# Performance work log

Measured on AMD Instinct MI355X. Metric: run time of the kernel, lower is better.

The kernel has to match this reference:

```python
import jax, jax.numpy as jnp
import numpy as np

EPS_NORM = 1e-6
EPS_LN = 1e-5


def setup_inputs() -> dict:
    key = jax.random.key(0)
    ks = jax.random.split(key, 6)
    b, m, d = 8, 1024, 768
    n, p = 64, 16
    h = 2 * d
    x = jax.random.normal(ks[0], (b, m, d), dtype=jnp.float32)
    phi = jax.random.normal(ks[1], (n, p, d), dtype=jnp.float32)
    # per-expert LayerNorm affine params
    ln_g = jnp.ones((n, d), dtype=jnp.float32)
    ln_b = jnp.zeros((n, d), dtype=jnp.float32)
    # per-expert MLP weights (torch Linear default init ~ U(-1/sqrt(fan_in), ...); use scaled normal)
    w1 = jax.random.normal(ks[2], (n, d, h), dtype=jnp.float32) * (1.0 / np.sqrt(d))
    b1 = jax.random.normal(ks[3], (n, h), dtype=jnp.float32) * 0.01
    w2 = jax.random.normal(ks[4], (n, h, d), dtype=jnp.float32) * (1.0 / np.sqrt(h))
    b2 = jax.random.normal(ks[5], (n, d), dtype=jnp.float32) * 0.01
    return {"x": x, "phi": phi, "ln_g": ln_g, "ln_b": ln_b,
            "w1": w1, "b1": b1, "w2": w2, "b2": b2}


def _layernorm(x, g, b):
    mu = jnp.mean(x, axis=-1, keepdims=True)
    var = jnp.mean(jnp.square(x - mu), axis=-1, keepdims=True)
    return (x - mu) * jax.lax.rsqrt(var + EPS_LN) * g + b


def reference(x, phi, ln_g, ln_b, w1, b1, w2, b2):
    # normalize phi over axis=0 (expert axis), as in the torch __init__
    phi_n = phi * jax.lax.rsqrt(jnp.sum(jnp.square(phi), axis=0, keepdims=True) + EPS_NORM)
    bsz, m, d = x.shape
    n, p, _ = phi_n.shape
    # routing logits: [b, m, n, p]
    logits = jnp.einsum('bmd,npd->bmnp', x, phi_n)
    # dispatch: softmax over tokens m
    D = jax.nn.softmax(logits, axis=1)
    # combine: softmax over flattened slots (n*p)
    C = jax.nn.softmax(logits.reshape(bsz, m, n * p), axis=-1)
    # input slots: [b, n, p, d]
    Xs = jnp.einsum('bmd,bmnp->bnpd', x, D)
    # batched per-expert MLP: LN -> Linear -> GELU -> Linear
    hdn = _layernorm(Xs, ln_g[:, None, :], ln_b[:, None, :])
    hdn = jnp.einsum('bnpd,ndh->bnph', hdn, w1) + b1[:, None, :]
    hdn = jax.nn.gelu(hdn, approximate=False)
    Ys = jnp.einsum('bnph,nhd->bnpd', hdn, w2) + b2[:, None, :]
    # combine: [b, m, d]
    Ys = Ys.reshape(bsz, n * p, d)
    Y = jnp.einsum('bsd,bms->bmd', Ys, C)
    return Y
```

## Files before the change

kernel.cpp:

```cpp
#include <hip/hip_runtime.h>
#include <math.h>

#define B 8
#define M 1024
#define D 768
#define NEXP 64
#define P 16
#define H 1536
#define S 1024
#define EPS_NORM 1e-6f
#define EPS_LN   1e-5f

typedef unsigned short u16;
typedef __attribute__((ext_vector_type(8))) short bf16x8;
typedef __attribute__((ext_vector_type(4))) float f32x4;

__device__ __forceinline__ u16 f2bf(float f) {
    union { float f; unsigned u; } v; v.f = f;
    unsigned r = v.u + 0x7FFFu + ((v.u >> 16) & 1u);
    return (u16)(r >> 16);
}

__device__ __forceinline__ float gelu_exact(float x) {
    return 0.5f * x * (1.0f + erff(x * 0.70710678118654752440f));
}

#define GLL16(g, l) __builtin_amdgcn_global_load_lds( \
    (const __attribute__((address_space(1))) void*)(g), \
    (__attribute__((address_space(3))) void*)(l), 16, 0, 0)

__device__ __forceinline__ void mfma_core_128(const u16* __restrict__ Ag,
                                              const u16* __restrict__ Bg,
                                              int K, u16* As, u16* Bs,
                                              f32x4 (&acc)[4][4]) {
    const int t    = threadIdx.x;
    const int lane = t & 63;
    const int wave = t >> 6;
    const int wr   = (wave >> 1) << 6;
    const int wc   = (wave & 1) << 6;
    const int quad = lane >> 4;
    const int l16  = lane & 15;
    const u16* ga0 = Ag + (size_t)(t >> 2) * K + (t & 3) * 8;
    const u16* ga1 = ga0 + (size_t)64 * K;
    const u16* gb0 = Bg + (size_t)(t >> 2) * K + (t & 3) * 8;
    const u16* gb1 = gb0 + (size_t)64 * K;
    u16* la0 = As + t * 8;
    u16* la1 = la0 + 2048;
    u16* lb0 = Bs + t * 8;
    u16* lb1 = lb0 + 2048;
    const u16* arp = As + (wr + l16) * 32 + quad * 8;
    const u16* brp = Bs + (wc + l16) * 32 + quad * 8;
    for (int k0 = 0; k0 < K; k0 += 32) {
        __syncthreads();
        GLL16(ga0 + k0, la0);
        GLL16(ga1 + k0, la1);
        GLL16(gb0 + k0, lb0);
        GLL16(gb1 + k0, lb1);
        __syncthreads();
        bf16x8 af[4], bfr[4];
#pragma unroll
        for (int i = 0; i < 4; ++i) af[i]  = *(const bf16x8*)(arp + i * 512);
#pragma unroll
        for (int j = 0; j < 4; ++j) bfr[j] = *(const bf16x8*)(brp + j * 512);
#pragma unroll
        for (int i = 0; i < 4; ++i)
#pragma unroll
            for (int j = 0; j < 4; ++j)
                acc[i][j] = __builtin_amdgcn_mfma_f32_16x16x32_bf16(af[i], bfr[j], acc[i][j], 0, 0, 0);
    }
}

#define EPI_VARS \
    const int t = threadIdx.x; const int lane = t & 63; const int wave = t >> 6; \
    const int wr = (wave >> 1) << 6; const int wc = (wave & 1) << 6; \
    const int quad = lane >> 4; const int l16 = lane & 15; (void)t;


__global__ __launch_bounds__(256) void cvt_x_kernel(const float* __restrict__ x,
                                                    u16* __restrict__ xb) {
    size_t i = ((size_t)blockIdx.x * 256 + threadIdx.x) * 4;
    float4 v = *(const float4*)(x + i);
    ushort4 o;
    o.x = f2bf(v.x); o.y = f2bf(v.y); o.z = f2bf(v.z); o.w = f2bf(v.w);
    *(ushort4*)(xb + i) = o;
}

__global__ __launch_bounds__(256) void phi_norm_kernel(const float* __restrict__ phi,
                                                       u16* __restrict__ phinb) {
    int pos = blockIdx.x * 256 + threadIdx.x;
    float ss = 0.f;
#pragma unroll 4
    for (int nn = 0; nn < NEXP; ++nn) {
        float v = phi[nn * (P*D) + pos];
        ss += v * v;
    }
    float r = rsqrtf(ss + EPS_NORM);
#pragma unroll 4
    for (int nn = 0; nn < NEXP; ++nn)
        phinb[nn * (P*D) + pos] = f2bf(phi[nn * (P*D) + pos] * r);
}

__global__ __launch_bounds__(256) void transpose_cvt_kernel(const float* __restrict__ in,
                                                            u16* __restrict__ out,
                                                            int R, int C,
                                                            size_t inStride, size_t outStride) {
    __shared__ float tile[64][65];
    const float* inb = in + (size_t)blockIdx.z * inStride;
    u16* outb = out + (size_t)blockIdx.z * outStride;
    int r0 = blockIdx.y * 64, c0 = blockIdx.x * 64;
    int tt = threadIdx.x;
    int rr = tt >> 4, c4 = (tt & 15) * 4;
#pragma unroll
    for (int i = 0; i < 4; ++i) {
        float4 v = *(const float4*)(inb + (size_t)(r0 + rr + i*16) * C + c0 + c4);
        tile[rr + i*16][c4 + 0] = v.x;
        tile[rr + i*16][c4 + 1] = v.y;
        tile[rr + i*16][c4 + 2] = v.z;
        tile[rr + i*16][c4 + 3] = v.w;
    }
    __syncthreads();
    int cr = tt >> 4, r4 = (tt & 15) * 4;
#pragma unroll
    for (int i = 0; i < 4; ++i) {
        int crow = cr + i * 16;
        ushort4 o;
        o.x = f2bf(tile[r4 + 0][crow]);
        o.y = f2bf(tile[r4 + 1][crow]);
        o.z = f2bf(tile[r4 + 2][crow]);
        o.w = f2bf(tile[r4 + 3][crow]);
        *(ushort4*)(outb + (size_t)(c0 + crow) * R + r0 + r4) = o;
    }
}


__global__ __launch_bounds__(256) void gemm_logits_mfma(const u16* __restrict__ xb,
                                                        const u16* __restrict__ phinb,
                                                        float* __restrict__ logits) {
    __shared__ __align__(16) u16 As[4096], Bs[4096];
    f32x4 acc[4][4];
#pragma unroll
    for (int i = 0; i < 4; ++i)
#pragma unroll
        for (int j = 0; j < 4; ++j) acc[i][j] = (f32x4){0.f, 0.f, 0.f, 0.f};
    const int row0 = blockIdx.y * 128, col0 = blockIdx.x * 128;
    mfma_core_128(xb + (size_t)row0 * D, phinb + (size_t)col0 * D, D, As, Bs, acc);
    EPI_VARS;
#pragma unroll
    for (int i = 0; i < 4; ++i)
#pragma unroll
        for (int j = 0; j < 4; ++j) {
            int col = col0 + wc + j*16 + l16;
#pragma unroll
            for (int r = 0; r < 4; ++r) {
                int row = row0 + wr + i*16 + quad*4 + r;
                logits[(size_t)row * S + col] = acc[i][j][r];
            }
        }
}

__global__ __launch_bounds__(256) void gemm_dispatch_mfma(const u16* __restrict__ DT,
                                                          const u16* __restrict__ xT,
                                                          float* __restrict__ Xs) {
    __shared__ __align__(16) u16 As[4096], Bs[4096];
    f32x4 acc[4][4];
#pragma unroll
    for (int i = 0; i < 4; ++i)
#pragma unroll
        for (int j = 0; j < 4; ++j) acc[i][j] = (f32x4){0.f, 0.f, 0.f, 0.f};
    const int b = blockIdx.z;
    const int row0 = blockIdx.y * 128, col0 = blockIdx.x * 128;
    mfma_core_128(DT + ((size_t)b * S + row0) * M,
                  xT + ((size_t)b * D + col0) * M, M, As, Bs, acc);
    EPI_VARS;
#pragma unroll
    for (int i = 0; i < 4; ++i)
#pragma unroll
        for (int j = 0; j < 4; ++j) {
            int col = col0 + wc + j*16 + l16;
#pragma unroll
            for (int r = 0; r < 4; ++r) {
                int row = row0 + wr + i*16 + quad*4 + r;
                Xs[((size_t)b * S + row) * D + col] = acc[i][j][r];
            }
        }
}

__global__ __launch_bounds__(256) void gemm_mlp1_mfma(const u16* __restrict__ hdnE,
                                                      const u16* __restrict__ w1T,
                                                      const float* __restrict__ b1,
                                                      u16* __restrict__ h1) {
    __shared__ __align__(16) u16 As[4096], Bs[4096];
    f32x4 acc[4][4];
#pragma unroll
    for (int i = 0; i < 4; ++i)
#pragma unroll
        for (int j = 0; j < 4; ++j) acc[i][j] = (f32x4){0.f, 0.f, 0.f, 0.f};
    const int n = blockIdx.z;
    const int col0 = blockIdx.x * 128;
    mfma_core_128(hdnE + (size_t)n * 128 * D,
                  w1T + ((size_t)n * H + col0) * D, D, As, Bs, acc);
    EPI_VARS;
#pragma unroll
    for (int i = 0; i < 4; ++i)
#pragma unroll
        for (int j = 0; j < 4; ++j) {
            int h = col0 + wc + j*16 + l16;
            float bias = b1[n * H + h];
#pragma unroll
            for (int r = 0; r < 4; ++r) {
                int row = wr + i*16 + quad*4 + r;
                h1[((size_t)n * 128 + row) * H + h] = f2bf(gelu_exact(acc[i][j][r] + bias));
            }
        }
}

__global__ __launch_bounds__(256) void gemm_mlp2_mfma(const u16* __restrict__ h1,
                                                      const u16* __restrict__ w2T,
                                                      const float* __restrict__ b2,
                                                      u16* __restrict__ YsT) {
    __shared__ __align__(16) u16 As[4096], Bs[4096];
    f32x4 acc[4][4];
#pragma unroll
    for (int i = 0; i < 4; ++i)
#pragma unroll
        for (int j = 0; j < 4; ++j) acc[i][j] = (f32x4){0.f, 0.f, 0.f, 0.f};
    const int n = blockIdx.z;
    const int col0 = blockIdx.x * 128;
    mfma_core_128(h1 + (size_t)n * 128 * H,
                  w2T + ((size_t)n * D + col0) * H, H, As, Bs, acc);
    EPI_VARS;
#pragma unroll
    for (int i = 0; i < 4; ++i)
#pragma unroll
        for (int j = 0; j < 4; ++j) {
            int d = col0 + wc + j*16 + l16;
            float bias = b2[n * D + d];
            int bb = ((wr + i*16) >> 4);
            int p0 = quad * 4;
            ushort4 o;
            o.x = f2bf(acc[i][j][0] + bias);
            o.y = f2bf(acc[i][j][1] + bias);
            o.z = f2bf(acc[i][j][2] + bias);
            o.w = f2bf(acc[i][j][3] + bias);
            *(ushort4*)(YsT + ((size_t)bb * D + d) * S + n * P + p0) = o;
        }
}

__global__ __launch_bounds__(256) void gemm_combine_mfma(const u16* __restrict__ Cb,
                                                         const u16* __restrict__ YsT,
                                                         float* __restrict__ out) {
    __shared__ __align__(16) u16 As[4096], Bs[4096];
    f32x4 acc[4][4];
#pragma unroll
    for (int i = 0; i < 4; ++i)
#pragma unroll
        for (int j = 0; j < 4; ++j) acc[i][j] = (f32x4){0.f, 0.f, 0.f, 0.f};
    const int b = blockIdx.z;
    const int row0 = blockIdx.y * 128, col0 = blockIdx.x * 128;
    mfma_core_128(Cb + ((size_t)b * M + row0) * S,
                  YsT + ((size_t)b * D + col0) * S, S, As, Bs, acc);
    EPI_VARS;
#pragma unroll
    for (int i = 0; i < 4; ++i)
#pragma unroll
        for (int j = 0; j < 4; ++j) {
            int col = col0 + wc + j*16 + l16;
#pragma unroll
            for (int r = 0; r < 4; ++r) {
                int row = row0 + wr + i*16 + quad*4 + r;
                out[((size_t)b * M + row) * D + col] = acc[i][j][r];
            }
        }
}


__global__ __launch_bounds__(256) void softmax_row_kernel(const float* __restrict__ in,
                                                          u16* __restrict__ outb) {
    __shared__ float red[4], red2[4];
    int row = blockIdx.x;
    int t = threadIdx.x;
    const float* rp = in + (size_t)row * S;
    float4 v = *(const float4*)(rp + t*4);
    float mx = fmaxf(fmaxf(v.x, v.y), fmaxf(v.z, v.w));
#pragma unroll
    for (int o = 1; o < 64; o <<= 1) mx = fmaxf(mx, __shfl_xor(mx, o));
    if ((t & 63) == 0) red[t >> 6] = mx;
    __syncthreads();
    mx = fmaxf(fmaxf(red[0], red[1]), fmaxf(red[2], red[3]));
    float4 e;
    e.x = expf(v.x - mx); e.y = expf(v.y - mx); e.z = expf(v.z - mx); e.w = expf(v.w - mx);
    float sum = e.x + e.y + e.z + e.w;
#pragma unroll
    for (int o = 1; o < 64; o <<= 1) sum += __shfl_xor(sum, o);
    if ((t & 63) == 0) red2[t >> 6] = sum;
    __syncthreads();
    sum = red2[0] + red2[1] + red2[2] + red2[3];
    float inv = 1.f / sum;
    ushort4 o4;
    o4.x = f2bf(e.x * inv); o4.y = f2bf(e.y * inv);
    o4.z = f2bf(e.z * inv); o4.w = f2bf(e.w * inv);
    *(ushort4*)(outb + (size_t)row * S + t*4) = o4;
}

__global__ __launch_bounds__(256) void colsm_partial_kernel(const float* __restrict__ logits,
                                                            float* __restrict__ pm,
                                                            float* __restrict__ pl) {
    int gid = blockIdx.x * 256 + threadIdx.x;
    int c   = gid >> 13;
    int col = gid & 8191;
    int b = col >> 10, s = col & (S - 1);
    const float* base = logits + ((size_t)b << 20) + ((size_t)(c * 128) << 10) + s;
    float mx = -INFINITY, l = 0.f;
    for (int m = 0; m < 128; ++m) {
        float v = base[(size_t)m << 10];
        float nm = fmaxf(mx, v);
        l = l * expf(mx - nm) + expf(v - nm);
        mx = nm;
    }
    pm[gid] = mx;
    pl[gid] = l;
}

__global__ __launch_bounds__(256) void colsm_combine_kernel(const float* __restrict__ pm,
                                                            const float* __restrict__ pl,
                                                            float* __restrict__ fm,
                                                            float* __restrict__ fl) {
    int col = blockIdx.x * 256 + threadIdx.x;
    float mx = -INFINITY;
#pragma unroll
    for (int c = 0; c < 8; ++c) mx = fmaxf(mx, pm[c * 8192 + col]);
    float l = 0.f;
#pragma unroll
    for (int c = 0; c < 8; ++c) l += pl[c * 8192 + col] * expf(pm[c * 8192 + col] - mx);
    fm[col] = mx;
    fl[col] = 1.f / l;
}

__global__ __launch_bounds__(256) void dt_transpose_kernel(const float* __restrict__ logits,
                                                           const float* __restrict__ fm,
                                                           const float* __restrict__ fl,
                                                           u16* __restrict__ DT) {
    __shared__ float tile[64][65];
    int b = blockIdx.z;
    int m0 = blockIdx.y * 64, s0 = blockIdx.x * 64;
    int tt = threadIdx.x;
    int rr = tt >> 4, c4 = (tt & 15) * 4;
    float4 fmv = *(const float4*)(fm + (size_t)b * S + s0 + c4);
    float4 flv = *(const float4*)(fl + (size_t)b * S + s0 + c4);
#pragma unroll
    for (int i = 0; i < 4; ++i) {
        float4 v = *(const float4*)(logits + ((size_t)b * M + m0 + rr + i*16) * S + s0 + c4);
        tile[rr + i*16][c4 + 0] = expf(v.x - fmv.x) * flv.x;
        tile[rr + i*16][c4 + 1] = expf(v.y - fmv.y) * flv.y;
        tile[rr + i*16][c4 + 2] = expf(v.z - fmv.z) * flv.z;
        tile[rr + i*16][c4 + 3] = expf(v.w - fmv.w) * flv.w;
    }
    __syncthreads();
    int cr = tt >> 4, r4 = (tt & 15) * 4;
#pragma unroll
    for (int i = 0; i < 4; ++i) {
        int crow = cr + i * 16;
        ushort4 o;
        o.x = f2bf(tile[r4 + 0][crow]);
        o.y = f2bf(tile[r4 + 1][crow]);
        o.z = f2bf(tile[r4 + 2][crow]);
        o.w = f2bf(tile[r4 + 3][crow]);
        *(ushort4*)(DT + ((size_t)b * S + s0 + crow) * M + m0 + r4) = o;
    }
}

__global__ __launch_bounds__(256) void layernorm_kernel(const float* __restrict__ Xs,
                                                        const float* __restrict__ g,
                                                        const float* __restrict__ bt,
                                                        u16* __restrict__ hdnE) {
    __shared__ float rs[4], rq[4];
    int row = blockIdx.x;
    int b = row >> 10;
    int n = (row >> 4) & (NEXP - 1);
    int p = row & 15;
    const float* rp = Xs + (size_t)row * D;
    u16* op = hdnE + ((size_t)n * 128 + b * 16 + p) * D;
    int t = threadIdx.x;
    float x0 = rp[t], x1 = rp[t + 256], x2 = rp[t + 512];
    float s  = x0 + x1 + x2;
    float sq = x0*x0 + x1*x1 + x2*x2;
#pragma unroll
    for (int o = 1; o < 64; o <<= 1) { s += __shfl_xor(s, o); sq += __shfl_xor(sq, o); }
    if ((t & 63) == 0) { rs[t >> 6] = s; rq[t >> 6] = sq; }
    __syncthreads();
    s  = rs[0] + rs[1] + rs[2] + rs[3];
    sq = rq[0] + rq[1] + rq[2] + rq[3];
    float mu  = s * (1.f / D);
    float var = sq * (1.f / D) - mu * mu;
    float inv = rsqrtf(var + EPS_LN);
    const float* gn = g  + n * D;
    const float* bn = bt + n * D;
    op[t]       = f2bf((x0 - mu) * inv * gn[t]       + bn[t]);
    op[t + 256] = f2bf((x1 - mu) * inv * gn[t + 256] + bn[t + 256]);
    op[t + 512] = f2bf((x2 - mu) * inv * gn[t + 512] + bn[t + 512]);
}

extern "C" void kernel_launch(void* const* d_in, const int* in_sizes, int n_in,
                              void* d_out, int out_size, void* d_ws, size_t ws_size,
                              hipStream_t stream) {
    const float* x    = (const float*)d_in[0];
    const float* phi  = (const float*)d_in[1];
    const float* ln_g = (const float*)d_in[2];
    const float* ln_b = (const float*)d_in[3];
    const float* w1   = (const float*)d_in[4];
    const float* b1   = (const float*)d_in[5];
    const float* w2   = (const float*)d_in[6];
    const float* b2   = (const float*)d_in[7];
    float* out = (float*)d_out;

    char* ws = (char*)d_ws;
    u16*   wT     = (u16*)(ws + 0);
    float* logits = (float*)(ws + 150994944);
    u16*   Cb     = (u16*)(ws + 184549376);
    u16*   xb     = (u16*)(ws + 201326592);
    u16*   DT     = (u16*)(ws + 213909504);
    u16*   xTb    = (u16*)(ws + 230686720);
    u16*   phinb  = (u16*)(ws + 243269632);
    u16*   hdnE   = (u16*)(ws + 244842496);
    float* pm     = (float*)(ws + 257425408);
    float* pl     = (float*)(ws + 257687552);
    float* fm     = (float*)(ws + 257949696);
    float* fl     = (float*)(ws + 257982464);
    float* Xs     = logits;
    u16*   h1     = xb;
    u16*   YsT    = xTb;

    cvt_x_kernel<<<6144, 256, 0, stream>>>(x, xb);
    phi_norm_kernel<<<48, 256, 0, stream>>>(phi, phinb);
    transpose_cvt_kernel<<<dim3(12, 16, B), 256, 0, stream>>>(
        x, xTb, M, D, (size_t)M * D, (size_t)D * M);
    transpose_cvt_kernel<<<dim3(24, 12, NEXP), 256, 0, stream>>>(
        w1, wT, D, H, (size_t)D * H, (size_t)H * D);

    gemm_logits_mfma<<<dim3(8, 64), 256, 0, stream>>>(xb, phinb, logits);
    softmax_row_kernel<<<B * M, 256, 0, stream>>>(logits, Cb);
    colsm_partial_kernel<<<256, 256, 0, stream>>>(logits, pm, pl);
    colsm_combine_kernel<<<32, 256, 0, stream>>>(pm, pl, fm, fl);
    dt_transpose_kernel<<<dim3(16, 16, B), 256, 0, stream>>>(logits, fm, fl, DT);

    gemm_dispatch_mfma<<<dim3(6, 8, B), 256, 0, stream>>>(DT, xTb, Xs);
    layernorm_kernel<<<B * S, 256, 0, stream>>>(Xs, ln_g, ln_b, hdnE);

    gemm_mlp1_mfma<<<dim3(12, 1, NEXP), 256, 0, stream>>>(hdnE, wT, b1, h1);
    transpose_cvt_kernel<<<dim3(12, 24, NEXP), 256, 0, stream>>>(
        w2, wT, H, D, (size_t)H * D, (size_t)D * H);
    gemm_mlp2_mfma<<<dim3(6, 1, NEXP), 256, 0, stream>>>(h1, wT, b2, YsT);

    gemm_combine_mfma<<<dim3(6, 8, B), 256, 0, stream>>>(Cb, YsT, out);
}
```

Before: 924.0 us.

## Fuse weight transpose-convert into MLP GEMMs and merge x prep kernels

The MLP GEMMs now read fp32 w1/w2 directly in their natural [K,N] layout, converting them to bf16 and transposing into padded shared memory inside the K loop. This removes the two separate transpose_cvt passes over 64 experts' weights, which wrote and re-read a large bf16 workspace. The x bf16 conversion and x transpose are also merged into one kernel that reads x once. In exchange, the B operand loads become strided fp32 scalar loads with in-loop conversion and no async copy, which may slow the GEMM inner loop.

```diff
diff --git a/kernel.cpp b/kernel.cpp
--- a/kernel.cpp
+++ b/kernel.cpp
@@ -70,19 +70,98 @@
     }
 }
 
+__device__ __forceinline__ void mfma_core_bf32(const u16* __restrict__ Ag, int K,
+                                               const float* __restrict__ Bg, int ldb,
+                                               u16* As, u16* Bs,
+                                               f32x4 (&acc)[4][4]) {
+    const int t    = threadIdx.x;
+    const int lane = t & 63;
+    const int wave = t >> 6;
+    const int wr   = (wave >> 1) << 6;
+    const int wc   = (wave & 1) << 6;
+    const int quad = lane >> 4;
+    const int l16  = lane & 15;
+    const u16* ga0 = Ag + (size_t)(t >> 2) * K + (t & 3) * 8;
+    const u16* ga1 = ga0 + (size_t)64 * K;
+    u16* la0 = As + t * 8;
+    u16* la1 = la0 + 2048;
+    const int bcol = t & 127;
+    const int kq   = (t >> 7) << 4;
+    const float* bg0 = Bg + (size_t)kq * ldb + bcol;
+    u16* lb = Bs + bcol * 40 + kq;
+    const u16* arp = As + (wr + l16) * 32 + quad * 8;
+    const u16* brp = Bs + (wc + l16) * 40 + quad * 8;
+    for (int k0 = 0; k0 < K; k0 += 32) {
+        const float* bg = bg0 + (size_t)k0 * ldb;
+        __syncthreads();
+        GLL16(ga0 + k0, la0);
+        GLL16(ga1 + k0, la1);
+        float f[16];
+#pragma unroll
+        for (int i = 0; i < 16; ++i) f[i] = bg[(size_t)i * ldb];
+#pragma unroll
+        for (int i = 0; i < 4; ++i) {
+            ushort4 o;
+            o.x = f2bf(f[i*4 + 0]); o.y = f2bf(f[i*4 + 1]);
+            o.z = f2bf(f[i*4 + 2]); o.w = f2bf(f[i*4 + 3]);
+            *(ushort4*)(lb + i * 4) = o;
+        }
+        __syncthreads();
+        bf16x8 af[4], bfr[4];
+#pragma unroll
+        for (int i = 0; i < 4; ++i) af[i]  = *(const bf16x8*)(arp + i * 512);
+#pragma unroll
+        for (int j = 0; j < 4; ++j) bfr[j] = *(const bf16x8*)(brp + j * 640);
+#pragma unroll
+        for (int i = 0; i < 4; ++i)
+#pragma unroll
+            for (int j = 0; j < 4; ++j)
+                acc[i][j] = __builtin_amdgcn_mfma_f32_16x16x32_bf16(af[i], bfr[j], acc[i][j], 0, 0, 0);
+    }
+}
+
 #define EPI_VARS \
     const int t = threadIdx.x; const int lane = t & 63; const int wave = t >> 6; \
     const int wr = (wave >> 1) << 6; const int wc = (wave & 1) << 6; \
     const int quad = lane >> 4; const int l16 = lane & 15; (void)t;
 
-
-__global__ __launch_bounds__(256) void cvt_x_kernel(const float* __restrict__ x,
-                                                    u16* __restrict__ xb) {
-    size_t i = ((size_t)blockIdx.x * 256 + threadIdx.x) * 4;
-    float4 v = *(const float4*)(x + i);
-    ushort4 o;
-    o.x = f2bf(v.x); o.y = f2bf(v.y); o.z = f2bf(v.z); o.w = f2bf(v.w);
-    *(ushort4*)(xb + i) = o;
+#define ACC_INIT \
+    f32x4 acc[4][4]; \
+    _Pragma("unroll") for (int i = 0; i < 4; ++i) \
+    _Pragma("unroll") for (int j = 0; j < 4; ++j) acc[i][j] = (f32x4){0.f, 0.f, 0.f, 0.f};
+
+__global__ __launch_bounds__(256) void xprep_kernel(const float* __restrict__ x,
+                                                    u16* __restrict__ xb,
+                                                    u16* __restrict__ xT) {
+    __shared__ float tile[64][65];
+    int b = blockIdx.z;
+    int m0 = blockIdx.y * 64, d0 = blockIdx.x * 64;
+    int tt = threadIdx.x;
+    int rr = tt >> 4, c4 = (tt & 15) * 4;
+#pragma unroll
+    for (int i = 0; i < 4; ++i) {
+        int m = m0 + rr + i * 16;
+        float4 v = *(const float4*)(x + ((size_t)b * M + m) * D + d0 + c4);
+        tile[rr + i*16][c4 + 0] = v.x;
+        tile[rr + i*16][c4 + 1] = v.y;
+        tile[rr + i*16][c4 + 2] = v.z;
+        tile[rr + i*16][c4 + 3] = v.w;
+        ushort4 o;
+        o.x = f2bf(v.x); o.y = f2bf(v.y); o.z = f2bf(v.z); o.w = f2bf(v.w);
+        *(ushort4*)(xb + ((size_t)b * M + m) * D + d0 + c4) = o;
+    }
+    __syncthreads();
+    int cr = tt >> 4, r4 = (tt & 15) * 4;
+#pragma unroll
+    for (int i = 0; i < 4; ++i) {
+        int crow = cr + i * 16;
+        ushort4 o;
+        o.x = f2bf(tile[r4 + 0][crow]);
+        o.y = f2bf(tile[r4 + 1][crow]);
+        o.z = f2bf(tile[r4 + 2][crow]);
+        o.w = f2bf(tile[r4 + 3][crow]);
+        *(ushort4*)(xT + ((size_t)b * D + d0 + crow) * M + m0 + r4) = o;
+    }
 }
 
 __global__ __launch_bounds__(256) void phi_norm_kernel(const float* __restrict__ phi,
@@ -100,48 +179,12 @@
         phinb[nn * (P*D) + pos] = f2bf(phi[nn * (P*D) + pos] * r);
 }
 
-__global__ __launch_bounds__(256) void transpose_cvt_kernel(const float* __restrict__ in,
-                                                            u16* __restrict__ out,
-                                                            int R, int C,
-                                                            size_t inStride, size_t outStride) {
-    __shared__ float tile[64][65];
-    const float* inb = in + (size_t)blockIdx.z * inStride;
-    u16* outb = out + (size_t)blockIdx.z * outStride;
-    int r0 = blockIdx.y * 64, c0 = blockIdx.x * 64;
-    int tt = threadIdx.x;
-    int rr = tt >> 4, c4 = (tt & 15) * 4;
-#pragma unroll
-    for (int i = 0; i < 4; ++i) {
-        float4 v = *(const float4*)(inb + (size_t)(r0 + rr + i*16) * C + c0 + c4);
-        tile[rr + i*16][c4 + 0] = v.x;
-        tile[rr + i*16][c4 + 1] = v.y;
-        tile[rr + i*16][c4 + 2] = v.z;
-        tile[rr + i*16][c4 + 3] = v.w;
-    }
-    __syncthreads();
-    int cr = tt >> 4, r4 = (tt & 15) * 4;
-#pragma unroll
-    for (int i = 0; i < 4; ++i) {
-        int crow = cr + i * 16;
-        ushort4 o;
-        o.x = f2bf(tile[r4 + 0][crow]);
-        o.y = f2bf(tile[r4 + 1][crow]);
-        o.z = f2bf(tile[r4 + 2][crow]);
-        o.w = f2bf(tile[r4 + 3][crow]);
-        *(ushort4*)(outb + (size_t)(c0 + crow) * R + r0 + r4) = o;
-    }
-}
-
 
 __global__ __launch_bounds__(256) void gemm_logits_mfma(const u16* __restrict__ xb,
                                                         const u16* __restrict__ phinb,
                                                         float* __restrict__ logits) {
     __shared__ __align__(16) u16 As[4096], Bs[4096];
-    f32x4 acc[4][4];
-#pragma unroll
-    for (int i = 0; i < 4; ++i)
-#pragma unroll
-        for (int j = 0; j < 4; ++j) acc[i][j] = (f32x4){0.f, 0.f, 0.f, 0.f};
+    ACC_INIT;
     const int row0 = blockIdx.y * 128, col0 = blockIdx.x * 128;
     mfma_core_128(xb + (size_t)row0 * D, phinb + (size_t)col0 * D, D, As, Bs, acc);
     EPI_VARS;
@@ -162,11 +205,7 @@
                                                           const u16* __restrict__ xT,
                                                           float* __restrict__ Xs) {
     __shared__ __align__(16) u16 As[4096], Bs[4096];
-    f32x4 acc[4][4];
-#pragma unroll
-    for (int i = 0; i < 4; ++i)
-#pragma unroll
-        for (int j = 0; j < 4; ++j) acc[i][j] = (f32x4){0.f, 0.f, 0.f, 0.f};
+    ACC_INIT;
     const int b = blockIdx.z;
     const int row0 = blockIdx.y * 128, col0 = blockIdx.x * 128;
     mfma_core_128(DT + ((size_t)b * S + row0) * M,
@@ -186,19 +225,15 @@
 }
 
 __global__ __launch_bounds__(256) void gemm_mlp1_mfma(const u16* __restrict__ hdnE,
-                                                      const u16* __restrict__ w1T,
+                                                      const float* __restrict__ w1,
                                                       const float* __restrict__ b1,
                                                       u16* __restrict__ h1) {
-    __shared__ __align__(16) u16 As[4096], Bs[4096];
-    f32x4 acc[4][4];
-#pragma unroll
-    for (int i = 0; i < 4; ++i)
-#pragma unroll
-        for (int j = 0; j < 4; ++j) acc[i][j] = (f32x4){0.f, 0.f, 0.f, 0.f};
+    __shared__ __align__(16) u16 As[4096], Bs[5120];
+    ACC_INIT;
     const int n = blockIdx.z;
     const int col0 = blockIdx.x * 128;
-    mfma_core_128(hdnE + (size_t)n * 128 * D,
-                  w1T + ((size_t)n * H + col0) * D, D, As, Bs, acc);
+    mfma_core_bf32(hdnE + (size_t)n * 128 * D, D,
+                   w1 + (size_t)n * D * H + col0, H, As, Bs, acc);
     EPI_VARS;
 #pragma unroll
     for (int i = 0; i < 4; ++i)
@@ -215,19 +250,15 @@
 }
 
 __global__ __launch_bounds__(256) void gemm_mlp2_mfma(const u16* __restrict__ h1,
-                                                      const u16* __restrict__ w2T,
+                                                      const float* __restrict__ w2,
                                                       const float* __restrict__ b2,
                                                       u16* __restrict__ YsT) {
-    __shared__ __align__(16) u16 As[4096], Bs[4096];
-    f32x4 acc[4][4];
-#pragma unroll
-    for (int i = 0; i < 4; ++i)
-#pragma unroll
-        for (int j = 0; j < 4; ++j) acc[i][j] = (f32x4){0.f, 0.f, 0.f, 0.f};
+    __shared__ __align__(16) u16 As[4096], Bs[5120];
+    ACC_INIT;
     const int n = blockIdx.z;
     const int col0 = blockIdx.x * 128;
-    mfma_core_128(h1 + (size_t)n * 128 * H,
-                  w2T + ((size_t)n * D + col0) * H, H, As, Bs, acc);
+    mfma_core_bf32(h1 + (size_t)n * 128 * H, H,
+                   w2 + (size_t)n * H * D + col0, D, As, Bs, acc);
     EPI_VARS;
 #pragma unroll
     for (int i = 0; i < 4; ++i)
@@ -250,11 +281,7 @@
                                                          const u16* __restrict__ YsT,
                                                          float* __restrict__ out) {
     __shared__ __align__(16) u16 As[4096], Bs[4096];
-    f32x4 acc[4][4];
-#pragma unroll
-    for (int i = 0; i < 4; ++i)
-#pragma unroll
-        for (int j = 0; j < 4; ++j) acc[i][j] = (f32x4){0.f, 0.f, 0.f, 0.f};
+    ACC_INIT;
     const int b = blockIdx.z;
     const int row0 = blockIdx.y * 128, col0 = blockIdx.x * 128;
     mfma_core_128(Cb + ((size_t)b * M + row0) * S,
@@ -414,28 +441,23 @@
     float* out = (float*)d_out;
 
     char* ws = (char*)d_ws;
-    u16*   wT     = (u16*)(ws + 0);
-    float* logits = (float*)(ws + 150994944);
-    u16*   Cb     = (u16*)(ws + 184549376);
-    u16*   xb     = (u16*)(ws + 201326592);
-    u16*   DT     = (u16*)(ws + 213909504);
-    u16*   xTb    = (u16*)(ws + 230686720);
-    u16*   phinb  = (u16*)(ws + 243269632);
-    u16*   hdnE   = (u16*)(ws + 244842496);
-    float* pm     = (float*)(ws + 257425408);
-    float* pl     = (float*)(ws + 257687552);
-    float* fm     = (float*)(ws + 257949696);
-    float* fl     = (float*)(ws + 257982464);
+    float* logits = (float*)(ws + 0);
+    u16*   Cb     = (u16*)(ws + 33554432);
+    u16*   xb     = (u16*)(ws + 50331648);
+    u16*   DT     = (u16*)(ws + 62914560);
+    u16*   xTb    = (u16*)(ws + 79691776);
+    u16*   phinb  = (u16*)(ws + 92274688);
+    u16*   hdnE   = (u16*)(ws + 93847552);
+    float* pm     = (float*)(ws + 106430464);
+    float* pl     = (float*)(ws + 106692608);
+    float* fm     = (float*)(ws + 106954752);
+    float* fl     = (float*)(ws + 106987520);
     float* Xs     = logits;
     u16*   h1     = xb;
     u16*   YsT    = xTb;
 
-    cvt_x_kernel<<<6144, 256, 0, stream>>>(x, xb);
+    xprep_kernel<<<dim3(12, 16, B), 256, 0, stream>>>(x, xb, xTb);
     phi_norm_kernel<<<48, 256, 0, stream>>>(phi, phinb);
-    transpose_cvt_kernel<<<dim3(12, 16, B), 256, 0, stream>>>(
-        x, xTb, M, D, (size_t)M * D, (size_t)D * M);
-    transpose_cvt_kernel<<<dim3(24, 12, NEXP), 256, 0, stream>>>(
-        w1, wT, D, H, (size_t)D * H, (size_t)H * D);
 
     gemm_logits_mfma<<<dim3(8, 64), 256, 0, stream>>>(xb, phinb, logits);
     softmax_row_kernel<<<B * M, 256, 0, stream>>>(logits, Cb);
@@ -446,10 +468,8 @@
     gemm_dispatch_mfma<<<dim3(6, 8, B), 256, 0, stream>>>(DT, xTb, Xs);
     layernorm_kernel<<<B * S, 256, 0, stream>>>(Xs, ln_g, ln_b, hdnE);
 
-    gemm_mlp1_mfma<<<dim3(12, 1, NEXP), 256, 0, stream>>>(hdnE, wT, b1, h1);
-    transpose_cvt_kernel<<<dim3(12, 24, NEXP), 256, 0, stream>>>(
-        w2, wT, H, D, (size_t)H * D, (size_t)D * H);
-    gemm_mlp2_mfma<<<dim3(6, 1, NEXP), 256, 0, stream>>>(h1, wT, b2, YsT);
+    gemm_mlp1_mfma<<<dim3(12, 1, NEXP), 256, 0, stream>>>(hdnE, w1, b1, h1);
+    gemm_mlp2_mfma<<<dim3(6, 1, NEXP), 256, 0, stream>>>(h1, w2, b2, YsT);
 
     gemm_combine_mfma<<<dim3(6, 8, B), 256, 0, stream>>>(Cb, YsT, out);
 }
```

Result: faster. 795.8 us (-13.9%).
